# Performance work log

Hardware: AMD Instinct MI355X
Metric: run time of the kernel (lower is better)

Reference implementation:

```python
import jax, jax.numpy as jnp
import numpy as np

N, E, G = 20000, 320000, 64
DIN, D, H, L = 256, 128, 4, 3
EPS = 1e-5
NEG_SLOPE = 0.2


def setup_inputs() -> dict:
    key = jax.random.key(0)
    ks = jax.random.split(key, 12)
    rn = lambda k, shape, s: jax.random.normal(k, shape, jnp.float32) * s
    x = jax.random.normal(ks[0], (N, DIN), jnp.float32)
    edge_index = jax.random.randint(ks[1], (2, E), 0, N, dtype=jnp.int32)
    batch = jnp.sort(jax.random.randint(ks[2], (N,), 0, G, dtype=jnp.int32))
    inp = {
        'x': x, 'edge_index': edge_index, 'batch': batch,
        'ip_w': rn(ks[3], (D, DIN), 1.0 / np.sqrt(DIN)), 'ip_b': jnp.zeros((D,), jnp.float32),
        'lin_w': rn(ks[4], (L, H * D, D), 1.0 / np.sqrt(D)),
        'att_src': rn(ks[5], (L, H, D), 0.1), 'att_dst': rn(ks[6], (L, H, D), 0.1),
        'gat_b': jnp.zeros((L, D), jnp.float32),
        'bn_g': jnp.ones((L, D), jnp.float32), 'bn_b': jnp.zeros((L, D), jnp.float32),
        'hw1': rn(ks[7], (3, D // 2, D), 1.0 / np.sqrt(D)), 'hb1': jnp.zeros((3, D // 2), jnp.float32),
        'hw2': rn(ks[8], (3, 1, D // 2), 1.0 / np.sqrt(D // 2)), 'hb2': jnp.zeros((3, 1), jnp.float32),
    }
    return inp


def _gat_layer(x, lin_w, att_src, att_dst, bias, src, dst):
    # x: [N, D] -> h: [N, H, D] per-head projected features
    h = (x @ lin_w.T).reshape(N, H, D)
    a_src = jnp.einsum('nhd,hd->nh', h, att_src)  # [N, H]
    a_dst = jnp.einsum('nhd,hd->nh', h, att_dst)
    e = jax.nn.leaky_relu(a_src[src] + a_dst[dst], NEG_SLOPE)  # [Etot, H]
    # segment softmax over edges grouped by destination node
    e_max = jax.ops.segment_max(e, dst, num_segments=N)
    w = jnp.exp(e - e_max[dst])
    denom = jax.ops.segment_sum(w, dst, num_segments=N)
    alpha = w / (denom[dst] + 1e-16)  # [Etot, H]
    msg = h[src] * alpha[:, :, None]  # [Etot, H, D]
    out = jax.ops.segment_sum(msg, dst, num_segments=N)  # [N, H, D]
    return out.mean(axis=1) + bias  # concat=False -> mean over heads


def _batch_norm(x, g, b):
    mu = x.mean(axis=0)
    var = x.var(axis=0)
    return (x - mu) * jax.lax.rsqrt(var + EPS) * g + b


def reference(x, edge_index, batch, ip_w, ip_b, lin_w, att_src, att_dst, gat_b,
              bn_g, bn_b, hw1, hb1, hw2, hb2):
    # add self loops (GATConv default)
    loop = jnp.arange(N, dtype=edge_index.dtype)
    src = jnp.concatenate([edge_index[0], loop])
    dst = jnp.concatenate([edge_index[1], loop])

    h = jax.nn.relu(x @ ip_w.T + ip_b)
    for l in range(L):
        h = _gat_layer(h, lin_w[l], att_src[l], att_dst[l], gat_b[l], src, dst)
        h = jax.nn.relu(_batch_norm(h, bn_g[l], bn_b[l]))
        # dropout: identity in eval mode

    # global mean pool over graphs
    sums = jax.ops.segment_sum(h, batch, num_segments=G)  # [G, D]
    cnt = jax.ops.segment_sum(jnp.ones((N,), h.dtype), batch, num_segments=G)
    pooled = sums / jnp.maximum(cnt, 1.0)[:, None]

    # three MLP heads (stacked): [3, G, D//2] -> [3, G, 1]
    hid = jax.nn.relu(jnp.einsum('gd,kod->kgo', pooled, hw1) + hb1[:, None, :])
    out = jnp.einsum('kgo,kpo->kgp', hid, hw2) + hb2[:, None, :]  # [3, G, 1]
    return jnp.transpose(out[:, :, 0])  # [G, 3] == cat([orig, quant, qat], dim=1)
```

## Files before the change

### kernel.cpp

```cpp
#include <hip/hip_runtime.h>
#include <math.h>

#define N_NODES 20000
#define N_EDGES 320000
#define ETOT    (N_EDGES + N_NODES)
#define NGRAPH  64
#define DIN     256
#define DD      128
#define NH      4
#define NL      3
#define HPD     (NH*DD)
#define EPS_BN  1e-5f
#define SLOPE   0.2f

typedef __attribute__((ext_vector_type(8))) short short8;
typedef __attribute__((ext_vector_type(4))) float f32x4;

__device__ __forceinline__ float lrelu(float x) { return x >= 0.f ? x : SLOPE * x; }

__device__ __forceinline__ unsigned short f2bf(float f) {
  unsigned u = __float_as_uint(f);
  unsigned r = (u + 0x7FFFu + ((u >> 16) & 1u)) >> 16;
  return (unsigned short)r;
}
__device__ __forceinline__ float bf2f(unsigned short b) {
  return __uint_as_float((unsigned)b << 16);
}
__device__ __forceinline__ void bf2x(unsigned u, float& lo, float& hi) {
  lo = __uint_as_float(u << 16);
  hi = __uint_as_float(u & 0xFFFF0000u);
}

__global__ void f2bf_kernel(const float* __restrict__ in, unsigned short* __restrict__ out, int n4) {
  int i = blockIdx.x * 256 + threadIdx.x;
  if (i >= n4) return;
  float4 v = *(const float4*)&in[(size_t)i * 4];
  ushort4 o;
  o.x = f2bf(v.x); o.y = f2bf(v.y); o.z = f2bf(v.z); o.w = f2bf(v.w);
  *(ushort4*)&out[(size_t)i * 4] = o;
}

__global__ void hist_kernel(const int* __restrict__ ei, int* __restrict__ hist) {
  int idx = blockIdx.x * 256 + threadIdx.x;
  if (idx >= ETOT) return;
  int d = (idx < N_EDGES) ? ei[N_EDGES + idx] : (idx - N_EDGES);
  atomicAdd(&hist[d], 1);
}

__global__ __launch_bounds__(1024) void scan_kernel(const int* __restrict__ hist,
                                                    int* __restrict__ offs,
                                                    int* __restrict__ cursor) {
  __shared__ int wsum[16];
  int tid = threadIdx.x, lane = tid & 63, wid = tid >> 6;
  int carry = 0;
  for (int base = 0; base < N_NODES; base += 1024) {
    int i = base + tid;
    int x = (i < N_NODES) ? hist[i] : 0;
    int v = x;
    #pragma unroll
    for (int d = 1; d < 64; d <<= 1) {
      int t = __shfl_up(v, d);
      if (lane >= d) v += t;
    }
    if (lane == 63) wsum[wid] = v;
    __syncthreads();
    if (wid == 0) {
      int sv = (lane < 16) ? wsum[lane] : 0;
      #pragma unroll
      for (int d = 1; d < 16; d <<= 1) {
        int t = __shfl_up(sv, d);
        if (lane >= d) sv += t;
      }
      if (lane < 16) wsum[lane] = sv;
    }
    __syncthreads();
    int woff = (wid > 0) ? wsum[wid - 1] : 0;
    int incl = carry + woff + v;
    if (i < N_NODES) { int e = incl - x; offs[i] = e; cursor[i] = e; }
    carry += wsum[15];
    __syncthreads();
  }
  if (tid == 0) offs[N_NODES] = carry;
}

__global__ void scatter_kernel(const int* __restrict__ ei, int* __restrict__ cursor,
                               int* __restrict__ esrc) {
  int idx = blockIdx.x * 256 + threadIdx.x;
  if (idx >= ETOT) return;
  int s, d;
  if (idx < N_EDGES) { s = ei[idx]; d = ei[N_EDGES + idx]; }
  else { s = idx - N_EDGES; d = s; }
  int pos = atomicAdd(&cursor[d], 1);
  esrc[pos] = s;
}

__global__ __launch_bounds__(256) void gemm_mfma_nt(
    const unsigned short* __restrict__ A,
    const unsigned short* __restrict__ B,
    unsigned short* __restrict__ Cb,
    int M, int Nc, int K,
    const float* __restrict__ bias, int do_relu)
{
  int lane = threadIdx.x & 63;
  int wid  = threadIdx.x >> 6;
  int wm = wid >> 1, wn = wid & 1;
  int m0 = blockIdx.y * 128 + wm * 64;
  int n0 = blockIdx.x * 128 + wn * 64;
  int lr = lane & 15;
  int kg = lane >> 4;

  f32x4 acc[4][4];
  #pragma unroll
  for (int i = 0; i < 4; ++i)
    #pragma unroll
    for (int j = 0; j < 4; ++j)
      acc[i][j] = (f32x4){0.f, 0.f, 0.f, 0.f};

  size_t abase[4], bbase[4];
  #pragma unroll
  for (int i = 0; i < 4; ++i) {
    int ar = m0 + i * 16 + lr;
    if (ar >= M) ar = M - 1;
    abase[i] = (size_t)ar * K;
    bbase[i] = (size_t)(n0 + i * 16 + lr) * K;
  }

  int nk = K >> 5;
  short8 afr[4], bfr[4], a2[4], b2[4];
  #pragma unroll
  for (int i = 0; i < 4; ++i) {
    afr[i] = *(const short8*)&A[abase[i] + kg * 8];
    bfr[i] = *(const short8*)&B[bbase[i] + kg * 8];
  }
  for (int ks = 0; ks < nk; ++ks) {
    if (ks + 1 < nk) {
      int ko = (ks + 1) * 32 + kg * 8;
      #pragma unroll
      for (int i = 0; i < 4; ++i) {
        a2[i] = *(const short8*)&A[abase[i] + ko];
        b2[i] = *(const short8*)&B[bbase[i] + ko];
      }
    }
    #pragma unroll
    for (int i = 0; i < 4; ++i)
      #pragma unroll
      for (int j = 0; j < 4; ++j)
        acc[i][j] = __builtin_amdgcn_mfma_f32_16x16x32_bf16(afr[i], bfr[j], acc[i][j], 0, 0, 0);
    if (ks + 1 < nk) {
      #pragma unroll
      for (int i = 0; i < 4; ++i) { afr[i] = a2[i]; bfr[i] = b2[i]; }
    }
  }

  float bz[4];
  #pragma unroll
  for (int j = 0; j < 4; ++j)
    bz[j] = bias ? bias[n0 + j * 16 + lr] : 0.f;
  #pragma unroll
  for (int i = 0; i < 4; ++i) {
    #pragma unroll
    for (int r = 0; r < 4; ++r) {
      int row = m0 + i * 16 + kg * 4 + r;
      if (row < M) {
        size_t rb = (size_t)row * Nc;
        #pragma unroll
        for (int j = 0; j < 4; ++j) {
          float v = acc[i][j][r] + bz[j];
          if (do_relu) v = fmaxf(v, 0.f);
          Cb[rb + n0 + j * 16 + lr] = f2bf(v);
        }
      }
    }
  }
}

__global__ __launch_bounds__(256) void gemm_mfma_k128(
    const unsigned short* __restrict__ A,
    const unsigned short* __restrict__ B,
    unsigned short* __restrict__ Cb,
    int M, int Nc)
{
  int lane = threadIdx.x & 63;
  int wid  = threadIdx.x >> 6;
  int wm = wid >> 1, wn = wid & 1;
  int m0 = blockIdx.y * 128 + wm * 64;
  int n0 = blockIdx.x * 128 + wn * 64;
  int lr = lane & 15;
  int kg = lane >> 4;

  const unsigned short* Ap[4];
  const unsigned short* Bp[4];
  #pragma unroll
  for (int i = 0; i < 4; ++i) {
    int ar = m0 + i * 16 + lr;
    if (ar >= M) ar = M - 1;
    Ap[i] = A + (size_t)ar * 128 + kg * 8;
    Bp[i] = B + (size_t)(n0 + i * 16 + lr) * 128 + kg * 8;
  }

  short8 a[4][4], b[4][4];
  #pragma unroll
  for (int ks = 0; ks < 4; ++ks)
    #pragma unroll
    for (int i = 0; i < 4; ++i) {
      a[ks][i] = *(const short8*)(Ap[i] + ks * 32);
      b[ks][i] = *(const short8*)(Bp[i] + ks * 32);
    }

  f32x4 acc[4][4];
  #pragma unroll
  for (int i = 0; i < 4; ++i)
    #pragma unroll
    for (int j = 0; j < 4; ++j)
      acc[i][j] = (f32x4){0.f, 0.f, 0.f, 0.f};

  #pragma unroll
  for (int ks = 0; ks < 4; ++ks)
    #pragma unroll
    for (int i = 0; i < 4; ++i)
      #pragma unroll
      for (int j = 0; j < 4; ++j)
        acc[i][j] = __builtin_amdgcn_mfma_f32_16x16x32_bf16(a[ks][i], b[ks][j], acc[i][j], 0, 0, 0);

  #pragma unroll
  for (int i = 0; i < 4; ++i) {
    #pragma unroll
    for (int r = 0; r < 4; ++r) {
      int row = m0 + i * 16 + kg * 4 + r;
      if (row < M) {
        size_t rb = (size_t)row * Nc;
        #pragma unroll
        for (int j = 0; j < 4; ++j)
          Cb[rb + n0 + j * 16 + lr] = f2bf(acc[i][j][r]);
      }
    }
  }
}

__global__ __launch_bounds__(256) void attn_dots(const unsigned short* __restrict__ HPh,
    const float* __restrict__ atts, const float* __restrict__ attd,
    float* __restrict__ a_s, float* __restrict__ a_d)
{
  int lane = threadIdx.x & 63;
  int n = blockIdx.x * 4 + (threadIdx.x >> 6);
  uint4 u = *(const uint4*)&HPh[(size_t)n * HPD + lane * 8];
  float p0, p1, p2, p3, p4, p5, p6, p7;
  bf2x(u.x, p0, p1); bf2x(u.y, p2, p3); bf2x(u.z, p4, p5); bf2x(u.w, p6, p7);
  const float4* wsv = (const float4*)&atts[lane * 8];
  float4 s0 = wsv[0], s1 = wsv[1];
  const float4* wdv = (const float4*)&attd[lane * 8];
  float4 d0 = wdv[0], d1 = wdv[1];
  float ps = p0*s0.x + p1*s0.y + p2*s0.z + p3*s0.w
           + p4*s1.x + p5*s1.y + p6*s1.z + p7*s1.w;
  float pd = p0*d0.x + p1*d0.y + p2*d0.z + p3*d0.w
           + p4*d1.x + p5*d1.y + p6*d1.z + p7*d1.w;
  #pragma unroll
  for (int m = 1; m <= 8; m <<= 1) {
    ps += __shfl_xor(ps, m);
    pd += __shfl_xor(pd, m);
  }
  if ((lane & 15) == 0) {
    int h = lane >> 4;
    a_s[n * NH + h] = ps;
    a_d[n * NH + h] = pd;
  }
}

__global__ __launch_bounds__(256) void aggregate(const unsigned short* __restrict__ HPh,
    const float* __restrict__ a_s, const float* __restrict__ a_d,
    const int* __restrict__ offs, const int* __restrict__ esrc,
    const float* __restrict__ gbias, float* __restrict__ hout)
{
  int lane = threadIdx.x & 63;
  int n = blockIdx.x * 4 + (threadIdx.x >> 6);
  int start = offs[n], end = offs[n + 1];
  float4 ad4 = *(const float4*)&a_d[n * NH];
  int hsel = lane >> 4;
  int di = lane * 8;

  float4 m4 = make_float4(-1e30f, -1e30f, -1e30f, -1e30f);
  for (int j = start + lane; j < end; j += 64) {
    int s = esrc[j];
    float4 as4 = *(const float4*)&a_s[s * NH];
    m4.x = fmaxf(m4.x, lrelu(as4.x + ad4.x));
    m4.y = fmaxf(m4.y, lrelu(as4.y + ad4.y));
    m4.z = fmaxf(m4.z, lrelu(as4.z + ad4.z));
    m4.w = fmaxf(m4.w, lrelu(as4.w + ad4.w));
  }
  #pragma unroll
  for (int m = 1; m < 64; m <<= 1) {
    m4.x = fmaxf(m4.x, __shfl_xor(m4.x, m));
    m4.y = fmaxf(m4.y, __shfl_xor(m4.y, m));
    m4.z = fmaxf(m4.z, __shfl_xor(m4.z, m));
    m4.w = fmaxf(m4.w, __shfl_xor(m4.w, m));
  }
  float mh = (lane & 32) ? ((lane & 16) ? m4.w : m4.z) : ((lane & 16) ? m4.y : m4.x);
  float ad = (lane & 32) ? ((lane & 16) ? ad4.w : ad4.z) : ((lane & 16) ? ad4.y : ad4.x);

  float wacc = 0.f;
  float a0=0,a1=0,a2=0,a3=0,a4=0,a5=0,a6=0,a7=0;
  int sl = lane & 48;
  for (int base = start; base < end; base += 16) {
    int e = lane & 15;
    int j = base + e;
    float w = 0.f; int s = 0;
    if (j < end) {
      s = esrc[j];
      float a = a_s[s * NH + hsel];
      w = __expf(lrelu(a + ad) - mh);
    }
    wacc += w;
    int cnt = min(16, end - base);
    int t = 0;
    for (; t + 3 < cnt; t += 4) {
      int s0 = __shfl(s, sl | t);
      int s1 = __shfl(s, sl | (t + 1));
      int s2 = __shfl(s, sl | (t + 2));
      int s3 = __shfl(s, sl | (t + 3));
      float w0 = __shfl(w, sl | t);
      float w1 = __shfl(w, sl | (t + 1));
      float w2 = __shfl(w, sl | (t + 2));
      float w3 = __shfl(w, sl | (t + 3));
      uint4 u0 = *(const uint4*)&HPh[(size_t)s0 * HPD + di];
      uint4 u1 = *(const uint4*)&HPh[(size_t)s1 * HPD + di];
      uint4 u2 = *(const uint4*)&HPh[(size_t)s2 * HPD + di];
      uint4 u3 = *(const uint4*)&HPh[(size_t)s3 * HPD + di];
      float f0, f1, f2, f3, f4, f5, f6, f7;
      bf2x(u0.x, f0, f1); bf2x(u0.y, f2, f3); bf2x(u0.z, f4, f5); bf2x(u0.w, f6, f7);
      a0 = fmaf(w0, f0, a0); a1 = fmaf(w0, f1, a1); a2 = fmaf(w0, f2, a2); a3 = fmaf(w0, f3, a3);
      a4 = fmaf(w0, f4, a4); a5 = fmaf(w0, f5, a5); a6 = fmaf(w0, f6, a6); a7 = fmaf(w0, f7, a7);
      bf2x(u1.x, f0, f1); bf2x(u1.y, f2, f3); bf2x(u1.z, f4, f5); bf2x(u1.w, f6, f7);
      a0 = fmaf(w1, f0, a0); a1 = fmaf(w1, f1, a1); a2 = fmaf(w1, f2, a2); a3 = fmaf(w1, f3, a3);
      a4 = fmaf(w1, f4, a4); a5 = fmaf(w1, f5, a5); a6 = fmaf(w1, f6, a6); a7 = fmaf(w1, f7, a7);
      bf2x(u2.x, f0, f1); bf2x(u2.y, f2, f3); bf2x(u2.z, f4, f5); bf2x(u2.w, f6, f7);
      a0 = fmaf(w2, f0, a0); a1 = fmaf(w2, f1, a1); a2 = fmaf(w2, f2, a2); a3 = fmaf(w2, f3, a3);
      a4 = fmaf(w2, f4, a4); a5 = fmaf(w2, f5, a5); a6 = fmaf(w2, f6, a6); a7 = fmaf(w2, f7, a7);
      bf2x(u3.x, f0, f1); bf2x(u3.y, f2, f3); bf2x(u3.z, f4, f5); bf2x(u3.w, f6, f7);
      a0 = fmaf(w3, f0, a0); a1 = fmaf(w3, f1, a1); a2 = fmaf(w3, f2, a2); a3 = fmaf(w3, f3, a3);
      a4 = fmaf(w3, f4, a4); a5 = fmaf(w3, f5, a5); a6 = fmaf(w3, f6, a6); a7 = fmaf(w3, f7, a7);
    }
    for (; t < cnt; ++t) {
      int sj = __shfl(s, sl | t);
      float wj = __shfl(w, sl | t);
      uint4 u = *(const uint4*)&HPh[(size_t)sj * HPD + di];
      float f0, f1, f2, f3, f4, f5, f6, f7;
      bf2x(u.x, f0, f1); bf2x(u.y, f2, f3); bf2x(u.z, f4, f5); bf2x(u.w, f6, f7);
      a0 = fmaf(wj, f0, a0); a1 = fmaf(wj, f1, a1); a2 = fmaf(wj, f2, a2); a3 = fmaf(wj, f3, a3);
      a4 = fmaf(wj, f4, a4); a5 = fmaf(wj, f5, a5); a6 = fmaf(wj, f6, a6); a7 = fmaf(wj, f7, a7);
    }
  }
  #pragma unroll
  for (int m = 1; m <= 8; m <<= 1) wacc += __shfl_xor(wacc, m);
  float inv = 1.f / (wacc + 1e-16f);
  float r0=a0*inv, r1=a1*inv, r2=a2*inv, r3=a3*inv;
  float r4=a4*inv, r5=a5*inv, r6=a6*inv, r7=a7*inv;
  #pragma unroll
  for (int m = 16; m <= 32; m <<= 1) {
    r0 += __shfl_xor(r0, m); r1 += __shfl_xor(r1, m);
    r2 += __shfl_xor(r2, m); r3 += __shfl_xor(r3, m);
    r4 += __shfl_xor(r4, m); r5 += __shfl_xor(r5, m);
    r6 += __shfl_xor(r6, m); r7 += __shfl_xor(r7, m);
  }
  if (lane < 16) {
    int dbase = lane * 8;
    const float4* gb = (const float4*)&gbias[dbase];
    float4 g0 = gb[0], g1 = gb[1];
    float4 o0 = make_float4(r0*0.25f + g0.x, r1*0.25f + g0.y, r2*0.25f + g0.z, r3*0.25f + g0.w);
    float4 o1 = make_float4(r4*0.25f + g1.x, r5*0.25f + g1.y, r6*0.25f + g1.z, r7*0.25f + g1.w);
    *(float4*)&hout[(size_t)n * DD + dbase] = o0;
    *(float4*)&hout[(size_t)n * DD + dbase + 4] = o1;
  }
}

__global__ __launch_bounds__(128) void bn_stats(const float* __restrict__ h,
    float* __restrict__ bs, float* __restrict__ bq)
{
  int c = threadIdx.x;
  float s = 0.f, q = 0.f;
  for (int r = blockIdx.x; r < N_NODES; r += gridDim.x) {
    float v = h[(size_t)r * DD + c];
    s += v; q = fmaf(v, v, q);
  }
  atomicAdd(&bs[c], s);
  atomicAdd(&bq[c], q);
}

__global__ __launch_bounds__(256) void bn_apply(const float* __restrict__ h,
    const float* __restrict__ bs, const float* __restrict__ bq,
    const float* __restrict__ g, const float* __restrict__ b,
    unsigned short* __restrict__ hbf)
{
  const float invN = 1.f / (float)N_NODES;
  int i4 = blockIdx.x * 256 + threadIdx.x;
  int c0 = (i4 * 4) & (DD - 1);
  float4 v = *(const float4*)&h[(size_t)i4 * 4];
  float4 s = *(const float4*)&bs[c0];
  float4 q = *(const float4*)&bq[c0];
  float4 gg = *(const float4*)&g[c0];
  float4 bb = *(const float4*)&b[c0];
  float mu, var;
  ushort4 o;
  mu = s.x * invN; var = q.x * invN - mu * mu;
  o.x = f2bf(fmaxf((v.x - mu) * rsqrtf(var + EPS_BN) * gg.x + bb.x, 0.f));
  mu = s.y * invN; var = q.y * invN - mu * mu;
  o.y = f2bf(fmaxf((v.y - mu) * rsqrtf(var + EPS_BN) * gg.y + bb.y, 0.f));
  mu = s.z * invN; var = q.z * invN - mu * mu;
  o.z = f2bf(fmaxf((v.z - mu) * rsqrtf(var + EPS_BN) * gg.z + bb.z, 0.f));
  mu = s.w * invN; var = q.w * invN - mu * mu;
  o.w = f2bf(fmaxf((v.w - mu) * rsqrtf(var + EPS_BN) * gg.w + bb.w, 0.f));
  *(ushort4*)&hbf[(size_t)i4 * 4] = o;
}

__global__ __launch_bounds__(256) void pool_partial(const unsigned short* __restrict__ hbf,
    const int* __restrict__ batch, float* __restrict__ psum)
{
  int g = blockIdx.x >> 3, sl = blockIdx.x & 7;
  int lo = 0, hi = N_NODES;
  while (lo < hi) { int mid = (lo + hi) >> 1; if (batch[mid] < g) lo = mid + 1; else hi = mid; }
  int start = lo;
  hi = N_NODES;
  while (lo < hi) { int mid = (lo + hi) >> 1; if (batch[mid] < g + 1) lo = mid + 1; else hi = mid; }
  int end = lo;
  int c = threadIdx.x & 127, ro = threadIdx.x >> 7;
  float s = 0.f;
  for (int r = start + sl * 2 + ro; r < end; r += 16) s += bf2f(hbf[(size_t)r * DD + c]);
  if (s != 0.f || true) atomicAdd(&psum[g * DD + c], s);
}

__global__ __launch_bounds__(64) void heads_kernel(const float* __restrict__ psum,
    const int* __restrict__ batch,
    const float* __restrict__ hw1, const float* __restrict__ hb1,
    const float* __restrict__ hw2, const float* __restrict__ hb2,
    float* __restrict__ out)
{
  int k = blockIdx.x >> 6;
  int g = blockIdx.x & 63;
  int o = threadIdx.x;
  int lo = 0, hi = N_NODES;
  while (lo < hi) { int mid = (lo + hi) >> 1; if (batch[mid] < g) lo = mid + 1; else hi = mid; }
  int start = lo;
  hi = N_NODES;
  while (lo < hi) { int mid = (lo + hi) >> 1; if (batch[mid] < g + 1) lo = mid + 1; else hi = mid; }
  float inv = 1.f / fmaxf((float)(lo - start), 1.f);
  const float4* p = (const float4*)&psum[g * DD];
  const float4* w = (const float4*)&hw1[((size_t)k * 64 + o) * DD];
  float dot = 0.f;
  #pragma unroll
  for (int d4 = 0; d4 < DD / 4; ++d4) {
    float4 pv = p[d4], wv = w[d4];
    dot += pv.x*wv.x + pv.y*wv.y + pv.z*wv.z + pv.w*wv.w;
  }
  float acc = fmaf(dot, inv, hb1[k * 64 + o]);
  float contrib = fmaxf(acc, 0.f) * hw2[k * 64 + o];
  #pragma unroll
  for (int m = 1; m < 64; m <<= 1) contrib += __shfl_xor(contrib, m);
  if (o == 0) out[g * 3 + k] = contrib + hb2[k];
}

extern "C" void kernel_launch(void* const* d_in, const int* in_sizes, int n_in,
                              void* d_out, int out_size, void* d_ws, size_t ws_size,
                              hipStream_t stream) {
  const float* x       = (const float*)d_in[0];
  const int*   ei      = (const int*)d_in[1];
  const int*   batch   = (const int*)d_in[2];
  const float* ip_w    = (const float*)d_in[3];
  const float* ip_b    = (const float*)d_in[4];
  const float* lin_w   = (const float*)d_in[5];
  const float* att_src = (const float*)d_in[6];
  const float* att_dst = (const float*)d_in[7];
  const float* gat_b   = (const float*)d_in[8];
  const float* bn_g    = (const float*)d_in[9];
  const float* bn_b    = (const float*)d_in[10];
  const float* hw1     = (const float*)d_in[11];
  const float* hb1     = (const float*)d_in[12];
  const float* hw2     = (const float*)d_in[13];
  const float* hb2     = (const float*)d_in[14];
  float* out = (float*)d_out;

  float* ws     = (float*)d_ws;
  float* hout   = ws;
  float* a_s    = hout + (size_t)N_NODES * DD;
  float* a_d    = a_s + (size_t)N_NODES * NH;
  float* bnsum  = a_d + (size_t)N_NODES * NH;
  float* bnss   = bnsum + NL * DD;
  float* pooled = bnss + NL * DD;
  unsigned short* HPh   = (unsigned short*)(pooled + NGRAPH * DD);
  unsigned short* xbf   = HPh;
  unsigned short* hbf   = HPh + (size_t)N_NODES * HPD;
  unsigned short* ipw_b = hbf + (size_t)N_NODES * DD;
  unsigned short* linw_b= ipw_b + DD * DIN;
  int*   hist   = (int*)(linw_b + (size_t)NL * HPD * DD);
  int*   offs   = hist + (N_NODES + 4);
  int*   cursor = offs + (N_NODES + 4);
  int*   esrc   = cursor + (N_NODES + 4);

  hipMemsetAsync(hist, 0, N_NODES * sizeof(int), stream);
  hipMemsetAsync(bnsum, 0, 2 * NL * DD * sizeof(float), stream);
  hipMemsetAsync(pooled, 0, NGRAPH * DD * sizeof(float), stream);

  f2bf_kernel<<<(DD * DIN / 4 + 255) / 256, 256, 0, stream>>>(ip_w, ipw_b, DD * DIN / 4);
  f2bf_kernel<<<(NL * HPD * DD / 4 + 255) / 256, 256, 0, stream>>>(lin_w, linw_b, NL * HPD * DD / 4);
  f2bf_kernel<<<(N_NODES * DIN / 4 + 255) / 256, 256, 0, stream>>>(x, xbf, N_NODES * DIN / 4);

  hist_kernel<<<(ETOT + 255) / 256, 256, 0, stream>>>(ei, hist);
  scan_kernel<<<1, 1024, 0, stream>>>(hist, offs, cursor);
  scatter_kernel<<<(ETOT + 255) / 256, 256, 0, stream>>>(ei, cursor, esrc);

  const int MB = (N_NODES + 127) / 128;

  gemm_mfma_nt<<<dim3(DD / 128, MB), 256, 0, stream>>>(
      xbf, ipw_b, hbf, N_NODES, DD, DIN, ip_b, 1);

  for (int l = 0; l < NL; ++l) {
    gemm_mfma_k128<<<dim3(HPD / 128, MB), 256, 0, stream>>>(
        hbf, linw_b + (size_t)l * HPD * DD, HPh, N_NODES, HPD);
    attn_dots<<<N_NODES / 4, 256, 0, stream>>>(
        HPh, att_src + (size_t)l * HPD, att_dst + (size_t)l * HPD, a_s, a_d);
    aggregate<<<N_NODES / 4, 256, 0, stream>>>(
        HPh, a_s, a_d, offs, esrc, gat_b + (size_t)l * DD, hout);
    bn_stats<<<256, 128, 0, stream>>>(hout, bnsum + l * DD, bnss + l * DD);
    bn_apply<<<(N_NODES * DD / 4) / 256, 256, 0, stream>>>(
        hout, bnsum + l * DD, bnss + l * DD, bn_g + (size_t)l * DD, bn_b + (size_t)l * DD, hbf);
  }

  pool_partial<<<NGRAPH * 8, 256, 0, stream>>>(hbf, batch, pooled);
  heads_kernel<<<NL * NGRAPH, 64, 0, stream>>>(pooled, batch, hw1, hb1, hw2, hb2, out);
}
```

Baseline: 478.1 us.

## Fuse x bf16 conversion into GEMM, parallelize scan, widen bn_stats

The input projection GEMM now reads fp32 x directly and packs it to bf16 in registers, removing the separate conversion kernel and its intermediate buffer. The single-block serial prefix scan is replaced by a three-kernel hierarchical scan across about 20 blocks. bn_stats uses 512 blocks of 256 threads with a shared-memory pre-reduction before the atomics. The GEMM now loads twice the bytes for A and adds conversion ALU work inside the loop, and the scan adds two extra launches.

```diff
diff --git a/kernel.cpp b/kernel.cpp
--- a/kernel.cpp
+++ b/kernel.cpp
@@ -12,6 +12,7 @@
 #define HPD     (NH*DD)
 #define EPS_BN  1e-5f
 #define SLOPE   0.2f
+#define SCAN_NB ((N_NODES + 1023) / 1024)
 
 typedef __attribute__((ext_vector_type(8))) short short8;
 typedef __attribute__((ext_vector_type(4))) float f32x4;
@@ -29,6 +30,14 @@
 __device__ __forceinline__ void bf2x(unsigned u, float& lo, float& hi) {
   lo = __uint_as_float(u << 16);
   hi = __uint_as_float(u & 0xFFFF0000u);
+}
+__device__ __forceinline__ short8 pack8(float4 a, float4 b) {
+  short8 r;
+  r[0] = (short)f2bf(a.x); r[1] = (short)f2bf(a.y);
+  r[2] = (short)f2bf(a.z); r[3] = (short)f2bf(a.w);
+  r[4] = (short)f2bf(b.x); r[5] = (short)f2bf(b.y);
+  r[6] = (short)f2bf(b.z); r[7] = (short)f2bf(b.w);
+  return r;
 }
 
 __global__ void f2bf_kernel(const float* __restrict__ in, unsigned short* __restrict__ out, int n4) {
@@ -47,40 +56,57 @@
   atomicAdd(&hist[d], 1);
 }
 
-__global__ __launch_bounds__(1024) void scan_kernel(const int* __restrict__ hist,
-                                                    int* __restrict__ offs,
-                                                    int* __restrict__ cursor) {
+__global__ __launch_bounds__(1024) void scan_blk(const int* __restrict__ hist,
+                                                 int* __restrict__ offs,
+                                                 int* __restrict__ bsum) {
   __shared__ int wsum[16];
   int tid = threadIdx.x, lane = tid & 63, wid = tid >> 6;
-  int carry = 0;
-  for (int base = 0; base < N_NODES; base += 1024) {
-    int i = base + tid;
-    int x = (i < N_NODES) ? hist[i] : 0;
-    int v = x;
-    #pragma unroll
-    for (int d = 1; d < 64; d <<= 1) {
-      int t = __shfl_up(v, d);
-      if (lane >= d) v += t;
-    }
-    if (lane == 63) wsum[wid] = v;
-    __syncthreads();
-    if (wid == 0) {
-      int sv = (lane < 16) ? wsum[lane] : 0;
-      #pragma unroll
-      for (int d = 1; d < 16; d <<= 1) {
-        int t = __shfl_up(sv, d);
-        if (lane >= d) sv += t;
-      }
-      if (lane < 16) wsum[lane] = sv;
-    }
-    __syncthreads();
-    int woff = (wid > 0) ? wsum[wid - 1] : 0;
-    int incl = carry + woff + v;
-    if (i < N_NODES) { int e = incl - x; offs[i] = e; cursor[i] = e; }
-    carry += wsum[15];
-    __syncthreads();
-  }
-  if (tid == 0) offs[N_NODES] = carry;
+  int i = blockIdx.x * 1024 + tid;
+  int x = (i < N_NODES) ? hist[i] : 0;
+  int v = x;
+  #pragma unroll
+  for (int d = 1; d < 64; d <<= 1) {
+    int t = __shfl_up(v, d);
+    if (lane >= d) v += t;
+  }
+  if (lane == 63) wsum[wid] = v;
+  __syncthreads();
+  if (wid == 0) {
+    int sv = (lane < 16) ? wsum[lane] : 0;
+    #pragma unroll
+    for (int d = 1; d < 16; d <<= 1) {
+      int t = __shfl_up(sv, d);
+      if (lane >= d) sv += t;
+    }
+    if (lane < 16) wsum[lane] = sv;
+  }
+  __syncthreads();
+  int woff = (wid > 0) ? wsum[wid - 1] : 0;
+  int incl = woff + v;
+  if (i < N_NODES) offs[i] = incl - x;
+  if (tid == 1023) bsum[blockIdx.x] = incl;
+}
+
+__global__ void scan_top(int* __restrict__ bsum, int* __restrict__ offs) {
+  int lane = threadIdx.x;
+  int v = (lane < SCAN_NB) ? bsum[lane] : 0;
+  int incl = v;
+  #pragma unroll
+  for (int d = 1; d < 64; d <<= 1) {
+    int t = __shfl_up(incl, d);
+    if (lane >= d) incl += t;
+  }
+  if (lane < SCAN_NB) bsum[lane] = incl - v;
+  if (lane == 63) offs[N_NODES] = incl;
+}
+
+__global__ void scan_fix(const int* __restrict__ bsum, int* __restrict__ offs,
+                         int* __restrict__ cursor) {
+  int i = blockIdx.x * 256 + threadIdx.x;
+  if (i >= N_NODES) return;
+  int v = offs[i] + bsum[i >> 10];
+  offs[i] = v;
+  cursor[i] = v;
 }
 
 __global__ void scatter_kernel(const int* __restrict__ ei, int* __restrict__ cursor,
@@ -94,8 +120,8 @@
   esrc[pos] = s;
 }
 
-__global__ __launch_bounds__(256) void gemm_mfma_nt(
-    const unsigned short* __restrict__ A,
+__global__ __launch_bounds__(256) void gemm_mfma_f32a(
+    const float* __restrict__ A,
     const unsigned short* __restrict__ B,
     unsigned short* __restrict__ Cb,
     int M, int Nc, int K,
@@ -126,10 +152,12 @@
   }
 
   int nk = K >> 5;
-  short8 afr[4], bfr[4], a2[4], b2[4];
+  float4 pa[4][2], na[4][2];
+  short8 bfr[4], b2[4];
   #pragma unroll
   for (int i = 0; i < 4; ++i) {
-    afr[i] = *(const short8*)&A[abase[i] + kg * 8];
+    pa[i][0] = *(const float4*)&A[abase[i] + kg * 8];
+    pa[i][1] = *(const float4*)&A[abase[i] + kg * 8 + 4];
     bfr[i] = *(const short8*)&B[bbase[i] + kg * 8];
   }
   for (int ks = 0; ks < nk; ++ks) {
@@ -137,18 +165,24 @@
       int ko = (ks + 1) * 32 + kg * 8;
       #pragma unroll
       for (int i = 0; i < 4; ++i) {
-        a2[i] = *(const short8*)&A[abase[i] + ko];
+        na[i][0] = *(const float4*)&A[abase[i] + ko];
+        na[i][1] = *(const float4*)&A[abase[i] + ko + 4];
         b2[i] = *(const short8*)&B[bbase[i] + ko];
       }
     }
+    short8 af[4];
+    #pragma unroll
+    for (int i = 0; i < 4; ++i) af[i] = pack8(pa[i][0], pa[i][1]);
     #pragma unroll
     for (int i = 0; i < 4; ++i)
       #pragma unroll
       for (int j = 0; j < 4; ++j)
-        acc[i][j] = __builtin_amdgcn_mfma_f32_16x16x32_bf16(afr[i], bfr[j], acc[i][j], 0, 0, 0);
+        acc[i][j] = __builtin_amdgcn_mfma_f32_16x16x32_bf16(af[i], bfr[j], acc[i][j], 0, 0, 0);
     if (ks + 1 < nk) {
       #pragma unroll
-      for (int i = 0; i < 4; ++i) { afr[i] = a2[i]; bfr[i] = b2[i]; }
+      for (int i = 0; i < 4; ++i) {
+        pa[i][0] = na[i][0]; pa[i][1] = na[i][1]; bfr[i] = b2[i];
+      }
     }
   }
 
@@ -372,17 +406,22 @@
   }
 }
 
-__global__ __launch_bounds__(128) void bn_stats(const float* __restrict__ h,
+__global__ __launch_bounds__(256) void bn_stats(const float* __restrict__ h,
     float* __restrict__ bs, float* __restrict__ bq)
 {
-  int c = threadIdx.x;
+  __shared__ float rs[256], rq[256];
+  int c = threadIdx.x & 127, ro = threadIdx.x >> 7;
   float s = 0.f, q = 0.f;
-  for (int r = blockIdx.x; r < N_NODES; r += gridDim.x) {
+  for (int r = blockIdx.x * 2 + ro; r < N_NODES; r += 1024) {
     float v = h[(size_t)r * DD + c];
     s += v; q = fmaf(v, v, q);
   }
-  atomicAdd(&bs[c], s);
-  atomicAdd(&bq[c], q);
+  rs[threadIdx.x] = s; rq[threadIdx.x] = q;
+  __syncthreads();
+  if (threadIdx.x < 128) {
+    atomicAdd(&bs[c], rs[c] + rs[c + 128]);
+    atomicAdd(&bq[c], rq[c] + rq[c + 128]);
+  }
 }
 
 __global__ __launch_bounds__(256) void bn_apply(const float* __restrict__ h,
@@ -424,7 +463,7 @@
   int c = threadIdx.x & 127, ro = threadIdx.x >> 7;
   float s = 0.f;
   for (int r = start + sl * 2 + ro; r < end; r += 16) s += bf2f(hbf[(size_t)r * DD + c]);
-  if (s != 0.f || true) atomicAdd(&psum[g * DD + c], s);
+  atomicAdd(&psum[g * DD + c], s);
 }
 
 __global__ __launch_bounds__(64) void heads_kernel(const float* __restrict__ psum,
@@ -485,7 +524,6 @@
   float* bnss   = bnsum + NL * DD;
   float* pooled = bnss + NL * DD;
   unsigned short* HPh   = (unsigned short*)(pooled + NGRAPH * DD);
-  unsigned short* xbf   = HPh;
   unsigned short* hbf   = HPh + (size_t)N_NODES * HPD;
   unsigned short* ipw_b = hbf + (size_t)N_NODES * DD;
   unsigned short* linw_b= ipw_b + DD * DIN;
@@ -493,6 +531,7 @@
   int*   offs   = hist + (N_NODES + 4);
   int*   cursor = offs + (N_NODES + 4);
   int*   esrc   = cursor + (N_NODES + 4);
+  int*   bsum   = esrc + ETOT + 4;
 
   hipMemsetAsync(hist, 0, N_NODES * sizeof(int), stream);
   hipMemsetAsync(bnsum, 0, 2 * NL * DD * sizeof(float), stream);
@@ -500,16 +539,17 @@
 
   f2bf_kernel<<<(DD * DIN / 4 + 255) / 256, 256, 0, stream>>>(ip_w, ipw_b, DD * DIN / 4);
   f2bf_kernel<<<(NL * HPD * DD / 4 + 255) / 256, 256, 0, stream>>>(lin_w, linw_b, NL * HPD * DD / 4);
-  f2bf_kernel<<<(N_NODES * DIN / 4 + 255) / 256, 256, 0, stream>>>(x, xbf, N_NODES * DIN / 4);
 
   hist_kernel<<<(ETOT + 255) / 256, 256, 0, stream>>>(ei, hist);
-  scan_kernel<<<1, 1024, 0, stream>>>(hist, offs, cursor);
+  scan_blk<<<SCAN_NB, 1024, 0, stream>>>(hist, offs, bsum);
+  scan_top<<<1, 64, 0, stream>>>(bsum, offs);
+  scan_fix<<<(N_NODES + 255) / 256, 256, 0, stream>>>(bsum, offs, cursor);
   scatter_kernel<<<(ETOT + 255) / 256, 256, 0, stream>>>(ei, cursor, esrc);
 
   const int MB = (N_NODES + 127) / 128;
 
-  gemm_mfma_nt<<<dim3(DD / 128, MB), 256, 0, stream>>>(
-      xbf, ipw_b, hbf, N_NODES, DD, DIN, ip_b, 1);
+  gemm_mfma_f32a<<<dim3(DD / 128, MB), 256, 0, stream>>>(
+      x, ipw_b, hbf, N_NODES, DD, DIN, ip_b, 1);
 
   for (int l = 0; l < NL; ++l) {
     gemm_mfma_k128<<<dim3(HPD / 128, MB), 256, 0, stream>>>(
@@ -518,7 +558,7 @@
         HPh, att_src + (size_t)l * HPD, att_dst + (size_t)l * HPD, a_s, a_d);
     aggregate<<<N_NODES / 4, 256, 0, stream>>>(
         HPh, a_s, a_d, offs, esrc, gat_b + (size_t)l * DD, hout);
-    bn_stats<<<256, 128, 0, stream>>>(hout, bnsum + l * DD, bnss + l * DD);
+    bn_stats<<<512, 256, 0, stream>>>(hout, bnsum + l * DD, bnss + l * DD);
     bn_apply<<<(N_NODES * DD / 4) / 256, 256, 0, stream>>>(
         hout, bnsum + l * DD, bnss + l * DD, bn_g + (size_t)l * DD, bn_b + (size_t)l * DD, hbf);
   }
```

Measured after the change: 443.4 us. 1.08x faster.
